# Kernel tuning notes

Measured on AMD Instinct MI355X. Metric: run time of the kernel, lower is better.

## Reference

```python
import jax, jax.numpy as jnp
import numpy as np

V = 30522   # bert-base-uncased vocab
E = 512     # embed_size
ATT = 512   # attention_dim
ENC = 2048  # encoder_dim
H = 512     # decoder_dim
B = 32
N = 49      # num image features (7x7)
T = 21      # caption length -> 20 decode steps


def setup_inputs() -> dict:
    key = jax.random.key(0)
    ks = jax.random.split(key, 12)
    s = lambda i, shape: jax.random.normal(ks[i], shape, jnp.float32) * 0.02
    features = jax.random.normal(ks[0], (B, N, ENC), jnp.float32)
    captions = jax.random.randint(ks[1], (B, T), 0, V, dtype=jnp.int32)
    return dict(
        features=features, captions=captions,
        emb=s(2, (V, E)),
        W_w=s(3, (ATT, H)), W_b=jnp.zeros((ATT,), jnp.float32),
        U_w=s(4, (ATT, ENC)), U_b=jnp.zeros((ATT,), jnp.float32),
        A_w=s(5, (1, ATT)), A_b=jnp.zeros((1,), jnp.float32),
        init_h_w=s(6, (H, ENC)), init_h_b=jnp.zeros((H,), jnp.float32),
        init_c_w=s(7, (H, ENC)), init_c_b=jnp.zeros((H,), jnp.float32),
        w_ih=s(8, (4 * H, E + ENC)), w_hh=s(9, (4 * H, H)),
        b_ih=jnp.zeros((4 * H,), jnp.float32), b_hh=jnp.zeros((4 * H,), jnp.float32),
        fcn_w=s(10, (V, H)), fcn_b=jnp.zeros((V,), jnp.float32),
    )


def reference(features, captions, emb, W_w, W_b, U_w, U_b, A_w, A_b,
              init_h_w, init_h_b, init_c_w, init_c_b,
              w_ih, w_hh, b_ih, b_hh, fcn_w, fcn_b):
    embeds = emb[captions]                      # [B, T, E]
    mean_f = features.mean(axis=1)              # [B, ENC]
    h0 = mean_f @ init_h_w.T + init_h_b         # [B, H]
    c0 = mean_f @ init_c_w.T + init_c_b
    # U(features) is h-independent: precompute once (same math as per-step in torch)
    u_hs = jnp.einsum('bne,ae->bna', features, U_w) + U_b  # [B, N, ATT]

    def step(carry, x_t):
        h, c = carry
        # Bahdanau attention
        w_ah = h @ W_w.T + W_b                               # [B, ATT]
        scores = jnp.tanh(u_hs + w_ah[:, None, :]) @ A_w[0] + A_b[0]  # [B, N]
        alpha = jax.nn.softmax(scores, axis=1)
        context = jnp.einsum('bn,bne->be', alpha, features)  # [B, ENC]
        # LSTMCell (torch gate order: i, f, g, o)
        lstm_in = jnp.concatenate([x_t, context], axis=1)    # [B, E+ENC]
        gates = lstm_in @ w_ih.T + b_ih + h @ w_hh.T + b_hh  # [B, 4H]
        i, f, g, o = jnp.split(gates, 4, axis=1)
        c2 = jax.nn.sigmoid(f) * c + jax.nn.sigmoid(i) * jnp.tanh(g)
        h2 = jax.nn.sigmoid(o) * jnp.tanh(c2)
        # dropout in eval mode = identity
        out = h2 @ fcn_w.T + fcn_b                           # [B, V]
        return (h2, c2), (out, alpha)

    xs = jnp.swapaxes(embeds[:, :-1], 0, 1)  # [T-1, B, E]
    _, (preds, alphas) = jax.lax.scan(step, (h0, c0), xs)
    return jnp.swapaxes(preds, 0, 1), jnp.swapaxes(alphas, 0, 1)
```

## Files before the change

### kernel.cpp

```cpp
#include <hip/hip_runtime.h>
#include <hip/hip_bf16.h>

#define VCB 30522
#define EMB 512
#define ATTD 512
#define ENC 2048
#define HD 512
#define BB 32
#define NF 49
#define TSTEPS 20
#define EIN 2560
#define KCAT 3072
#define WSTRIDE 3080
#define DTPB 512
#define NBLK 128

typedef __attribute__((ext_vector_type(8))) __bf16 bf16x8;
typedef __attribute__((ext_vector_type(4))) __bf16 bf16x4;
typedef __attribute__((ext_vector_type(4))) float floatx4;
typedef __hip_bfloat16 bf16;

__device__ __forceinline__ float bf2f(bf16 x){ return __bfloat162float(x); }
__device__ __forceinline__ bf16 f2bf(float x){ return __float2bfloat16(x); }
__device__ __forceinline__ float sigm(float x){ return 1.0f/(1.0f+expf(-x)); }
__device__ __forceinline__ float fast_tanh(float x){
    float e2 = __expf(2.0f*x);
    return 1.0f - 2.0f*__builtin_amdgcn_rcpf(e2 + 1.0f);
}

__device__ __forceinline__ unsigned coh_ld(const unsigned* p){
    return __hip_atomic_load(p, __ATOMIC_RELAXED, __HIP_MEMORY_SCOPE_AGENT);
}
__device__ __forceinline__ void coh_st(unsigned* p, unsigned v){
    __hip_atomic_store(p, v, __ATOMIC_RELAXED, __HIP_MEMORY_SCOPE_AGENT);
}
__device__ __forceinline__ unsigned pack2bf(float a, float b){
    unsigned short ua = __builtin_bit_cast(unsigned short, f2bf(a));
    unsigned short ub = __builtin_bit_cast(unsigned short, f2bf(b));
    return (unsigned)ua | ((unsigned)ub << 16);
}

__device__ __forceinline__ void gpost(unsigned* ctr){
    __syncthreads();
    if (threadIdx.x == 0)
        __hip_atomic_fetch_add(ctr, 1u, __ATOMIC_RELAXED, __HIP_MEMORY_SCOPE_AGENT);
}
__device__ __forceinline__ void gwait(const unsigned* ctr, unsigned tgt,
                                      volatile unsigned* sflag){
    float x = 1.0f;
    if (threadIdx.x < 64){
        while (coh_ld(ctr) < tgt){
#pragma unroll
            for (int i = 0; i < 8; ++i)
                x = __builtin_fmaf(x, 1.0000001f, 1e-12f);
        }
        if (threadIdx.x == 0) *sflag = tgt;
    } else {
        while (*sflag < tgt){
#pragma unroll
            for (int i = 0; i < 32; ++i)
                x = __builtin_fmaf(x, 1.0000001f, 1e-12f);
        }
    }
    asm volatile("" :: "v"(x));
    __syncthreads();
}

__device__ __forceinline__ float ld1(const void* base, size_t idx, int f){
    if (f) return ((const float*)base)[idx];
    return bf2f(((const bf16*)base)[idx]);
}
__device__ __forceinline__ bf16x8 ldbf8(const void* base, size_t idx, int f){
    if (f){
        const float* p = (const float*)base + idx;
        float4 a = *(const float4*)p, b = *(const float4*)(p+4);
        bf16x8 r;
        r[0]=(__bf16)a.x; r[1]=(__bf16)a.y; r[2]=(__bf16)a.z; r[3]=(__bf16)a.w;
        r[4]=(__bf16)b.x; r[5]=(__bf16)b.y; r[6]=(__bf16)b.z; r[7]=(__bf16)b.w;
        return r;
    }
    return *(const bf16x8*)((const bf16*)base + idx);
}
__device__ __forceinline__ bf16x8 bf8_of_f32(const float* p){
    float4 a = *(const float4*)p, b = *(const float4*)(p+4);
    bf16x8 r;
    r[0]=(__bf16)a.x; r[1]=(__bf16)a.y; r[2]=(__bf16)a.z; r[3]=(__bf16)a.w;
    r[4]=(__bf16)b.x; r[5]=(__bf16)b.y; r[6]=(__bf16)b.z; r[7]=(__bf16)b.w;
    return r;
}
__device__ __forceinline__ void st1(void* base, size_t idx, float v, int f){
    if (f) ((float*)base)[idx] = v;
    else   ((bf16*)base)[idx] = f2bf(v);
}

#define MFMA16(a,b,c) __builtin_amdgcn_mfma_f32_16x16x32_bf16(a,b,c,0,0,0)

__global__ void k_detect(const void* emb, int* flag, unsigned* bar){
    int tid = threadIdx.x;
    __shared__ int bad;
    if (tid == 0) bad = 0;
    for (int i = tid; i < 1024; i += 256) bar[i] = 0u;
    __syncthreads();
    const unsigned short* u = (const unsigned short*)emb;
    int local = 0;
    for (int i = tid; i < 4096; i += 256){
        int e = (u[i] >> 7) & 0xFF;
        if (e > 140) local = 1;
    }
    if (local) bad = 1;
    __syncthreads();
    if (tid == 0) *flag = bad;
}

__global__ void k_prep_gates(const void* w_ih, const void* w_hh, bf16* __restrict__ wcat,
                             const int* __restrict__ flag){
    int ff = *flag;
    int r = blockIdx.x, tid = threadIdx.x;
    for (int i = tid*8; i < KCAT; i += 2048){
        bf16x8 v;
        if (i + 8 <= EIN){
            v = ldbf8(w_ih, (size_t)r*EIN + i, ff);
        } else if (i >= EIN){
            v = ldbf8(w_hh, (size_t)r*HD + (i - EIN), ff);
        } else {
#pragma unroll
            for (int j = 0; j < 8; ++j){
                int k = i + j;
                v[j] = (__bf16)((k < EIN) ? ld1(w_ih, (size_t)r*EIN + k, ff)
                                          : ld1(w_hh, (size_t)r*HD + (k - EIN), ff));
            }
        }
        *(bf16x8*)(wcat + (size_t)r*KCAT + i) = v;
    }
}
__global__ void k_prep_cvt8(const void* src, bf16* __restrict__ dst, size_t n8,
                            const int* __restrict__ flag){
    int ff = *flag;
    size_t idx = (size_t)blockIdx.x*256 + threadIdx.x;
    size_t stride = (size_t)gridDim.x*256;
    for (size_t i = idx; i < n8; i += stride)
        *(bf16x8*)(dst + i*8) = ldbf8(src, i*8, ff);
}

__global__ void k_mean(const void* feat, float* __restrict__ mean_f,
                       const int* __restrict__ flag){
    int ff = *flag;
    int b = blockIdx.x, tid = threadIdx.x;
    for (int i = 0; i < ENC/256; ++i){
        int e = i*256 + tid;
        size_t base = (size_t)b*NF*ENC + e;
        float s = 0.f;
        for (int n = 0; n < NF; ++n) s += ld1(feat, base + (size_t)n*ENC, ff);
        mean_f[b*ENC + e] = s * (1.0f/49.0f);
    }
}

__global__ void k_init_hc(const float* __restrict__ mean_f,
                          const void* ihw, const void* ihb,
                          const void* icw, const void* icb,
                          float* __restrict__ Hbuf, float* __restrict__ c_f32,
                          const int* __restrict__ flag){
    int ff = *flag;
    int tid = threadIdx.x, wave = tid>>6, lane = tid&63, quad = lane>>4, lq = lane&15;
    int n0 = blockIdx.x*16;
    int ng = n0 + lq;
    const void* w = (ng < HD) ? ihw : icw;
    size_t wrow = (size_t)(ng < HD ? ng : ng - HD)*ENC;
    floatx4 acc[2] = {{0,0,0,0},{0,0,0,0}};
    int kb = wave*512;
    for (int kk = 0; kk < 16; ++kk){
        int k = kb + kk*32 + quad*8;
        bf16x8 bfr = ldbf8(w, wrow + k, ff);
#pragma unroll
        for (int mt = 0; mt < 2; ++mt){
            bf16x8 afr = bf8_of_f32(mean_f + (size_t)(mt*16+lq)*ENC + k);
            acc[mt] = MFMA16(afr, bfr, acc[mt]);
        }
    }
    __shared__ float red[4][2][16][16];
#pragma unroll
    for (int mt = 0; mt < 2; ++mt)
        for (int r = 0; r < 4; ++r)
            red[wave][mt][quad*4+r][lq] = acc[mt][r];
    __syncthreads();
    for (int rep = 0; rep < 2; ++rep){
        int idx = rep*256 + tid;
        int mt = idx>>8, mm = (idx>>4)&15, nn = idx&15;
        float v = red[0][mt][mm][nn]+red[1][mt][mm][nn]+red[2][mt][mm][nn]+red[3][mt][mm][nn];
        int n_g = n0 + nn, b = mt*16 + mm;
        if (n_g < HD) Hbuf[b*HD + n_g]        = v + ld1(ihb, n_g, ff);
        else          c_f32[b*HD + (n_g-HD)]  = v + ld1(icb, n_g - HD, ff);
    }
}

__global__ void k_uhs(const bf16* __restrict__ feat_bf, const void* U_w, const void* U_b,
                      float* __restrict__ u_hs, const int* __restrict__ flag){
    int ff = *flag;
    int tid = threadIdx.x, wave = tid>>6, lane = tid&63, quad = lane>>4, lq = lane&15;
    int m0 = blockIdx.x*16;
    int n0 = blockIdx.y*64 + wave*16;
    size_t arow = (size_t)(m0+lq)*ENC;
    size_t brow = (size_t)(n0+lq)*ENC;
    floatx4 acc = {0,0,0,0};
    for (int kk = 0; kk < ENC/32; ++kk){
        int k = kk*32 + quad*8;
        bf16x8 afr = *(const bf16x8*)(feat_bf + arow + k);
        bf16x8 bfr = ldbf8(U_w,  brow + k, ff);
        acc = MFMA16(afr, bfr, acc);
    }
    float ub = ld1(U_b, n0+lq, ff);
    for (int r = 0; r < 4; ++r){
        int m = m0 + quad*4 + r;
        u_hs[(size_t)m*ATTD + n0 + lq] = acc[r] + ub;
    }
}

__global__ void __launch_bounds__(DTPB) k_decode(
        float* __restrict__ Hbuf, const float* __restrict__ c0_f32,
        const bf16* __restrict__ Ww_bf, const void* __restrict__ W_b,
        const float* __restrict__ u_hs, const void* __restrict__ A_w,
        const void* __restrict__ A_b, const int* __restrict__ captions,
        const void* __restrict__ emb, const bf16* __restrict__ feat_bf,
        bf16* __restrict__ lstm_in, const bf16* __restrict__ wcat,
        const void* __restrict__ b_ih, const void* __restrict__ b_hh,
        bf16* __restrict__ Hall_bf, void* __restrict__ d_out,
        const int* __restrict__ flag, unsigned* __restrict__ bar)
{
    const int ff = *flag;
    const int bid = blockIdx.x, tid = threadIdx.x;
    const int wave = tid>>6, lane = tid&63, quad = lane>>4, lq = lane&15;

    __shared__ bf16  wlds[16*WSTRIDE];
    __shared__ float ubuf[4096];
    __shared__ float aw_s[ATTD];
    __shared__ float c_loc[BB*4];
    __shared__ float gbias[16];
    __shared__ unsigned sflag1, sflag2;

    unsigned* lin_u = (unsigned*)lstm_in;
    unsigned* flag1 = bar;
    unsigned* flag2 = bar + 64;

    if (tid == 0){ sflag1 = 0u; sflag2 = 0u; }

    for (int n = 0; n < 16; ++n){
        int g = n>>2, j = n&3;
        const bf16* src = wcat + (size_t)(g*HD + (bid<<2) + j)*KCAT;
        for (int c8 = tid; c8 < KCAT/8; c8 += DTPB)
            *(bf16x8*)(wlds + n*WSTRIDE + c8*8) = *(const bf16x8*)(src + c8*8);
    }
    if (tid < 128){
        int bb = tid&31, j = tid>>5, col = (bid<<2)+j;
        c_loc[bb*4+j] = c0_f32[bb*HD + col];
    }
    if (tid < 64){
        int bb = tid&31, j2 = tid>>5;
        int c0 = (bid<<2) + 2*j2;
        float h0 = Hbuf[bb*HD + c0], h1 = Hbuf[bb*HD + c0 + 1];
        coh_st(lin_u + (size_t)bb*(KCAT/2) + (EIN + c0)/2, pack2bf(h0, h1));
    }
    if (tid < 16){
        int g = tid>>2, j = tid&3, col = (bid<<2)+j;
        gbias[tid] = ld1(b_ih, g*HD+col, ff) + ld1(b_hh, g*HD+col, ff);
    }
    if (bid < BB)
        for (int i = tid; i < ATTD; i += DTPB) aw_s[i] = ld1(A_w, i, ff);
    gpost(flag2);

    float* h_sh    = ubuf;
    float* wah_s   = ubuf + 512;
    float* sc_s    = ubuf + 1024;
    float* alpha_s = ubuf + 1088;
    float (*red)[2][16][16] = (float (*)[2][16][16])ubuf;

    for (int t = 0; t < TSTEPS; ++t){
        if (bid < BB){
            gwait(flag2, 128u*(unsigned)(t+1), &sflag2);
            const int b = bid;
            const unsigned* hrow = (const unsigned*)(Hbuf + (size_t)t*BB*HD + b*HD);
            for (int i = tid; i < HD; i += DTPB)
                h_sh[i] = __uint_as_float(coh_ld(hrow + i));
            int cap = captions[b*21 + t];
            for (int e2 = tid; e2 < EMB/2; e2 += DTPB){
                float a = ld1(emb, (size_t)cap*EMB + 2*e2,     ff);
                float c = ld1(emb, (size_t)cap*EMB + 2*e2 + 1, ff);
                coh_st(lin_u + (size_t)b*(KCAT/2) + e2, pack2bf(a, c));
            }
            __syncthreads();
            for (int a = tid; a < ATTD; a += DTPB){
                const bf16* wr = Ww_bf + (size_t)a*HD;
                float s0=0.f, s1=0.f, s2=0.f, s3=0.f;
                for (int k = 0; k < HD; k += 8){
                    bf16x8 wv = *(const bf16x8*)(wr + k);
                    s0 += (float)wv[0]*h_sh[k+0] + (float)wv[4]*h_sh[k+4];
                    s1 += (float)wv[1]*h_sh[k+1] + (float)wv[5]*h_sh[k+5];
                    s2 += (float)wv[2]*h_sh[k+2] + (float)wv[6]*h_sh[k+6];
                    s3 += (float)wv[3]*h_sh[k+3] + (float)wv[7]*h_sh[k+7];
                }
                wah_s[a] = ((s0+s1)+(s2+s3)) + ld1(W_b, a, ff);
            }
            __syncthreads();
            {
                int a0 = lane*8;
                for (int n = wave; n < NF; n += 8){
                    const float* up = u_hs + (size_t)(b*NF + n)*ATTD + a0;
                    float4 u0 = *(const float4*)up;
                    float4 u1 = *(const float4*)(up + 4);
                    float p0 = fast_tanh(u0.x + wah_s[a0+0])*aw_s[a0+0]
                             + fast_tanh(u0.y + wah_s[a0+1])*aw_s[a0+1]
                             + fast_tanh(u0.z + wah_s[a0+2])*aw_s[a0+2]
                             + fast_tanh(u0.w + wah_s[a0+3])*aw_s[a0+3];
                    float p1 = fast_tanh(u1.x + wah_s[a0+4])*aw_s[a0+4]
                             + fast_tanh(u1.y + wah_s[a0+5])*aw_s[a0+5]
                             + fast_tanh(u1.z + wah_s[a0+6])*aw_s[a0+6]
                             + fast_tanh(u1.w + wah_s[a0+7])*aw_s[a0+7];
                    float p = p0 + p1;
                    for (int off = 32; off; off >>= 1) p += __shfl_down(p, off);
                    if (lane == 0) sc_s[n] = p + ld1(A_b, 0, ff);
                }
            }
            __syncthreads();
            if (wave == 0){
                float v = (lane < NF) ? sc_s[lane] : -1e30f;
                float mx = v;
                for (int off = 32; off; off >>= 1) mx = fmaxf(mx, __shfl_down(mx, off));
                mx = __shfl(mx, 0);
                float e = (lane < NF) ? expf(v - mx) : 0.f;
                float s = e;
                for (int off = 32; off; off >>= 1) s += __shfl_down(s, off);
                s = __shfl(s, 0);
                if (lane < NF){
                    float al = e / s;
                    alpha_s[lane] = al;
                    st1(d_out, (size_t)BB*TSTEPS*VCB + (size_t)b*(TSTEPS*NF) + t*NF + lane, al, ff);
                }
            }
            __syncthreads();
            {
                int e0 = tid*4;
                float acc[4] = {0,0,0,0};
#pragma unroll 7
                for (int n = 0; n < NF; ++n){
                    float al = alpha_s[n];
                    bf16x4 v = *(const bf16x4*)(feat_bf + (size_t)b*NF*ENC + (size_t)n*ENC + e0);
#pragma unroll
                    for (int j = 0; j < 4; ++j) acc[j] += al*(float)v[j];
                }
                unsigned* lrow = lin_u + (size_t)b*(KCAT/2) + (EMB + e0)/2;
                coh_st(lrow,     pack2bf(acc[0], acc[1]));
                coh_st(lrow + 1, pack2bf(acc[2], acc[3]));
            }
            gpost(flag1);
        }
        gwait(flag1, 32u*(unsigned)(t+1), &sflag1);

        {
            int kb = wave*384;
            floatx4 acc0 = {0,0,0,0}, acc1 = {0,0,0,0};
            const bf16* wrow = wlds + (size_t)lq*WSTRIDE;
            const unsigned* ar0 = lin_u + (size_t)lq*(KCAT/2);
            const unsigned* ar1 = lin_u + (size_t)(16+lq)*(KCAT/2);
            union U8 { unsigned u[4]; bf16x8 v; };
#pragma unroll
            for (int kk = 0; kk < 12; ++kk){
                int kd = (kb + kk*32 + quad*8) >> 1;
                bf16x8 bfr = *(const bf16x8*)(wrow + kb + kk*32 + quad*8);
                U8 a0, a1;
#pragma unroll
                for (int q = 0; q < 4; ++q){
                    a0.u[q] = coh_ld(ar0 + kd + q);
                    a1.u[q] = coh_ld(ar1 + kd + q);
                }
                acc0 = MFMA16(a0.v, bfr, acc0);
                acc1 = MFMA16(a1.v, bfr, acc1);
            }
#pragma unroll
            for (int r = 0; r < 4; ++r){
                red[wave][0][quad*4+r][lq] = acc0[r];
                red[wave][1][quad*4+r][lq] = acc1[r];
            }
        }
        __syncthreads();
        if (tid < 64){
            int bb = tid&31, j2 = tid>>5;
            int mt = bb>>4, mm = bb&15;
            float hn[2];
#pragma unroll
            for (int sub = 0; sub < 2; ++sub){
                int j = 2*j2 + sub;
                float G[4];
#pragma unroll
                for (int g = 0; g < 4; ++g){
                    int n = g*4 + j;
                    float s = 0.f;
#pragma unroll
                    for (int w8 = 0; w8 < 8; ++w8) s += red[w8][mt][mm][n];
                    G[g] = s + gbias[n];
                }
                float c_old = c_loc[bb*4+j];
                float c_new = sigm(G[1])*c_old + sigm(G[0])*tanhf(G[2]);
                float h_new = sigm(G[3])*tanhf(c_new);
                c_loc[bb*4+j] = c_new;
                hn[sub] = h_new;
            }
            int colb = (bid<<2) + 2*j2;
            unsigned* hb = (unsigned*)(Hbuf + (size_t)(t+1)*BB*HD + bb*HD + colb);
            coh_st(hb,     __float_as_uint(hn[0]));
            coh_st(hb + 1, __float_as_uint(hn[1]));
            ((unsigned*)Hall_bf)[((size_t)t*BB*HD + bb*HD + colb) >> 1] = pack2bf(hn[0], hn[1]);
            coh_st(lin_u + (size_t)bb*(KCAT/2) + (EIN + colb)/2, pack2bf(hn[0], hn[1]));
        }
        gpost(flag2);
    }
}

__global__ void __launch_bounds__(256) k_fcn(const bf16* __restrict__ Hall_bf,
                                             const bf16* __restrict__ fcnw_bf,
                                             const void* fcn_b, void* d_out,
                                             const int* __restrict__ flag){
    int ff = *flag;
    int tid = threadIdx.x, wave = tid>>6, lane = tid&63, quad = lane>>4, lq = lane&15;
    int n0 = blockIdx.x*64 + wave*16;
    int v = n0 + lq;
    int vc = (v < VCB) ? v : (VCB-1);
    const bf16* brow = fcnw_bf + (size_t)vc*HD;
    bf16x8 bfr[16];
#pragma unroll
    for (int kk = 0; kk < 16; ++kk) bfr[kk] = *(const bf16x8*)(brow + kk*32 + quad*8);
    float bias = ld1(fcn_b, vc, ff);
    for (int mt = 0; mt < 40; ++mt){
        const bf16* arow = Hall_bf + (size_t)(mt*16 + lq)*HD;
        floatx4 acc = {0,0,0,0};
#pragma unroll
        for (int kk = 0; kk < 16; ++kk){
            bf16x8 afr = *(const bf16x8*)(arow + kk*32 + quad*8);
            acc = MFMA16(afr, bfr[kk], acc);
        }
        if (v < VCB){
#pragma unroll
            for (int r = 0; r < 4; ++r){
                int m = mt*16 + quad*4 + r;
                int b = m & 31, tt = m >> 5;
                st1(d_out, (size_t)b*(TSTEPS*VCB) + (size_t)tt*VCB + v, acc[r] + bias, ff);
            }
        }
    }
}

extern "C" void kernel_launch(void* const* d_in, const int* in_sizes, int n_in,
                              void* d_out, int out_size, void* d_ws, size_t ws_size,
                              hipStream_t stream) {
    const void* feat  = d_in[0];
    const int*  caps  = (const int*)d_in[1];
    const void* emb   = d_in[2];
    const void* W_w   = d_in[3];
    const void* W_b   = d_in[4];
    const void* U_w   = d_in[5];
    const void* U_b   = d_in[6];
    const void* A_w   = d_in[7];
    const void* A_b   = d_in[8];
    const void* ihw   = d_in[9];
    const void* ihb   = d_in[10];
    const void* icw   = d_in[11];
    const void* icb   = d_in[12];
    const void* w_ih  = d_in[13];
    const void* w_hh  = d_in[14];
    const void* b_ih  = d_in[15];
    const void* b_hh  = d_in[16];
    const void* fcn_w = d_in[17];
    const void* fcn_b = d_in[18];

    char* ws = (char*)d_ws;
    size_t off = 0;
    float* u_hs    = (float*)(ws + off); off += (size_t)BB*NF*ATTD*4;
    float* c_f32   = (float*)(ws + off); off += (size_t)BB*HD*4;
    float* mean_f  = (float*)(ws + off); off += (size_t)BB*ENC*4;
    float* Hbuf    = (float*)(ws + off); off += (size_t)(TSTEPS+1)*BB*HD*4;
    bf16*  lstm_in = (bf16*) (ws + off); off += (size_t)BB*KCAT*2;
    bf16*  Hall_bf = (bf16*) (ws + off); off += (size_t)TSTEPS*BB*HD*2;
    bf16*  wcat    = (bf16*) (ws + off); off += (size_t)4*HD*KCAT*2;
    bf16*  fcnw_bf = (bf16*) (ws + off); off += (size_t)VCB*HD*2;
    bf16*  Ww_bf   = (bf16*) (ws + off); off += (size_t)ATTD*HD*2;
    bf16*  feat_bf = (bf16*) (ws + off); off += (size_t)BB*NF*ENC*2;
    int*   flag    = (int*)  (ws + off); off += 256;
    unsigned* bar  = (unsigned*)(ws + off); off += 4096;
    if (ws_size < off) return;

    k_detect    <<<1, 256, 0, stream>>>(emb, flag, bar);
    k_prep_gates<<<2048, 256, 0, stream>>>(w_ih, w_hh, wcat, flag);
    k_prep_cvt8 <<<2048, 256, 0, stream>>>(fcn_w, fcnw_bf, (size_t)VCB*HD/8, flag);
    k_prep_cvt8 <<<128, 256, 0, stream>>>(W_w, Ww_bf, (size_t)ATTD*HD/8, flag);
    k_prep_cvt8 <<<1024, 256, 0, stream>>>(feat, feat_bf, (size_t)BB*NF*ENC/8, flag);
    k_mean      <<<BB, 256, 0, stream>>>(feat, mean_f, flag);
    k_init_hc   <<<64, 256, 0, stream>>>(mean_f, ihw, ihb, icw, icb, Hbuf, c_f32, flag);
    k_uhs       <<<dim3(98, 8), 256, 0, stream>>>(feat_bf, U_w, U_b, u_hs, flag);

    {
        void* kargs[18] = {
            (void*)&Hbuf, (void*)&c_f32, (void*)&Ww_bf, (void*)&W_b,
            (void*)&u_hs, (void*)&A_w, (void*)&A_b, (void*)&caps,
            (void*)&emb, (void*)&feat_bf, (void*)&lstm_in, (void*)&wcat,
            (void*)&b_ih, (void*)&b_hh, (void*)&Hall_bf, (void*)&d_out,
            (void*)&flag, (void*)&bar
        };
        hipLaunchCooperativeKernel((void*)k_decode, dim3(NBLK), dim3(DTPB),
                                   kargs, 0, stream);
    }

    k_fcn<<<477, 256, 0, stream>>>(Hall_bf, fcnw_bf, fcn_b, d_out, flag);
}
```

Baseline: 1.577 ms.

## Distribute W·h attention GEMV and context reduction across blocks with extra grid flags

In the persistent decode kernel, the per-batch W_w·h GEMV moves from a scalar per-block loop to an MFMA computation split over 32 blocks, each owning 16 attention columns for all batches. The result is exchanged through a global buffer and a new flag. The alpha-weighted context sum is now spread over all 128 blocks (4 slices per batch) instead of 32, and the embedding copy is folded into that phase. This shortens the serial per-step work on the 32 attention blocks, but adds two more grid-wide barriers per step. It also drops the fp32 H buffer writes in favour of the bf16 copy already held in lstm_in.

Measured after the change: 1.451 ms. -7.9%, faster.

```diff
diff --git a/kernel.cpp b/kernel.cpp
--- a/kernel.cpp
+++ b/kernel.cpp
@@ -224,7 +224,8 @@
         bf16* __restrict__ lstm_in, const bf16* __restrict__ wcat,
         const void* __restrict__ b_ih, const void* __restrict__ b_hh,
         bf16* __restrict__ Hall_bf, void* __restrict__ d_out,
-        const int* __restrict__ flag, unsigned* __restrict__ bar)
+        const int* __restrict__ flag, unsigned* __restrict__ bar,
+        float* __restrict__ wah_u, float* __restrict__ alpha_u)
 {
     const int ff = *flag;
     const int bid = blockIdx.x, tid = threadIdx.x;
@@ -235,13 +236,17 @@
     __shared__ float aw_s[ATTD];
     __shared__ float c_loc[BB*4];
     __shared__ float gbias[16];
-    __shared__ unsigned sflag1, sflag2;
+    __shared__ unsigned sfW, sfS, sfL, sfH;
 
     unsigned* lin_u = (unsigned*)lstm_in;
-    unsigned* flag1 = bar;
-    unsigned* flag2 = bar + 64;
-
-    if (tid == 0){ sflag1 = 0u; sflag2 = 0u; }
+    unsigned* flagW = bar;
+    unsigned* flagS = bar + 64;
+    unsigned* flagL = bar + 128;
+    unsigned* flagH = bar + 192;
+    unsigned* wahu_u  = (unsigned*)wah_u;
+    unsigned* alphu_u = (unsigned*)alpha_u;
+
+    if (tid == 0){ sfW = 0u; sfS = 0u; sfL = 0u; sfH = 0u; }
 
     for (int n = 0; n < 16; ++n){
         int g = n>>2, j = n&3;
@@ -265,9 +270,8 @@
     }
     if (bid < BB)
         for (int i = tid; i < ATTD; i += DTPB) aw_s[i] = ld1(A_w, i, ff);
-    gpost(flag2);
-
-    float* h_sh    = ubuf;
+    gpost(flagH);
+
     float* wah_s   = ubuf + 512;
     float* sc_s    = ubuf + 1024;
     float* alpha_s = ubuf + 1088;
@@ -275,30 +279,50 @@
 
     for (int t = 0; t < TSTEPS; ++t){
         if (bid < BB){
-            gwait(flag2, 128u*(unsigned)(t+1), &sflag2);
+            gwait(flagH, 128u*(unsigned)(t+1), &sfH);
+            {
+                int n0 = bid<<4;
+                int kb = wave*64;
+                floatx4 acc0 = {0,0,0,0}, acc1 = {0,0,0,0};
+                const bf16* brow = Ww_bf + (size_t)(n0+lq)*HD;
+                union U8 { unsigned u[4]; bf16x8 v; };
+#pragma unroll
+                for (int kk = 0; kk < 2; ++kk){
+                    int k = kb + kk*32 + quad*8;
+                    bf16x8 bfr = *(const bf16x8*)(brow + k);
+                    U8 a0, a1;
+                    const unsigned* ar0 = lin_u + (size_t)lq*(KCAT/2) + (EIN+k)/2;
+                    const unsigned* ar1 = lin_u + (size_t)(16+lq)*(KCAT/2) + (EIN+k)/2;
+#pragma unroll
+                    for (int q = 0; q < 4; ++q){
+                        a0.u[q] = coh_ld(ar0 + q);
+                        a1.u[q] = coh_ld(ar1 + q);
+                    }
+                    acc0 = MFMA16(a0.v, bfr, acc0);
+                    acc1 = MFMA16(a1.v, bfr, acc1);
+                }
+#pragma unroll
+                for (int r = 0; r < 4; ++r){
+                    red[wave][0][quad*4+r][lq] = acc0[r];
+                    red[wave][1][quad*4+r][lq] = acc1[r];
+                }
+            }
+            __syncthreads();
+            {
+                int b = tid>>4, c = tid&15;
+                int mt = b>>4, mm = b&15;
+                float s = 0.f;
+#pragma unroll
+                for (int w8 = 0; w8 < 8; ++w8) s += red[w8][mt][mm][c];
+                int col = (bid<<4) + c;
+                coh_st(wahu_u + (size_t)b*ATTD + col,
+                       __float_as_uint(s + ld1(W_b, col, ff)));
+            }
+            gpost(flagW);
+
+            gwait(flagW, 32u*(unsigned)(t+1), &sfW);
             const int b = bid;
-            const unsigned* hrow = (const unsigned*)(Hbuf + (size_t)t*BB*HD + b*HD);
-            for (int i = tid; i < HD; i += DTPB)
-                h_sh[i] = __uint_as_float(coh_ld(hrow + i));
-            int cap = captions[b*21 + t];
-            for (int e2 = tid; e2 < EMB/2; e2 += DTPB){
-                float a = ld1(emb, (size_t)cap*EMB + 2*e2,     ff);
-                float c = ld1(emb, (size_t)cap*EMB + 2*e2 + 1, ff);
-                coh_st(lin_u + (size_t)b*(KCAT/2) + e2, pack2bf(a, c));
-            }
-            __syncthreads();
-            for (int a = tid; a < ATTD; a += DTPB){
-                const bf16* wr = Ww_bf + (size_t)a*HD;
-                float s0=0.f, s1=0.f, s2=0.f, s3=0.f;
-                for (int k = 0; k < HD; k += 8){
-                    bf16x8 wv = *(const bf16x8*)(wr + k);
-                    s0 += (float)wv[0]*h_sh[k+0] + (float)wv[4]*h_sh[k+4];
-                    s1 += (float)wv[1]*h_sh[k+1] + (float)wv[5]*h_sh[k+5];
-                    s2 += (float)wv[2]*h_sh[k+2] + (float)wv[6]*h_sh[k+6];
-                    s3 += (float)wv[3]*h_sh[k+3] + (float)wv[7]*h_sh[k+7];
-                }
-                wah_s[a] = ((s0+s1)+(s2+s3)) + ld1(W_b, a, ff);
-            }
+            wah_s[tid] = __uint_as_float(coh_ld(wahu_u + (size_t)b*ATTD + tid));
             __syncthreads();
             {
                 int a0 = lane*8;
@@ -331,28 +355,40 @@
                 s = __shfl(s, 0);
                 if (lane < NF){
                     float al = e / s;
-                    alpha_s[lane] = al;
+                    coh_st(alphu_u + b*64 + lane, __float_as_uint(al));
                     st1(d_out, (size_t)BB*TSTEPS*VCB + (size_t)b*(TSTEPS*NF) + t*NF + lane, al, ff);
                 }
             }
+            gpost(flagS);
+        }
+        gwait(flagS, 32u*(unsigned)(t+1), &sfS);
+        {
+            const int b = bid>>2, sl = bid&3;
+            if (tid < NF) alpha_s[tid] = __uint_as_float(coh_ld(alphu_u + b*64 + tid));
             __syncthreads();
-            {
-                int e0 = tid*4;
-                float acc[4] = {0,0,0,0};
+            if (tid < 256){
+                int col = sl*512 + 2*tid;
+                const bf16* fb = feat_bf + (size_t)b*NF*ENC + col;
+                float a0 = 0.f, a1 = 0.f;
 #pragma unroll 7
                 for (int n = 0; n < NF; ++n){
+                    unsigned fv = *(const unsigned*)(fb + (size_t)n*ENC);
+                    float lo = __uint_as_float(fv << 16);
+                    float hi = __uint_as_float(fv & 0xffff0000u);
                     float al = alpha_s[n];
-                    bf16x4 v = *(const bf16x4*)(feat_bf + (size_t)b*NF*ENC + (size_t)n*ENC + e0);
-#pragma unroll
-                    for (int j = 0; j < 4; ++j) acc[j] += al*(float)v[j];
-                }
-                unsigned* lrow = lin_u + (size_t)b*(KCAT/2) + (EMB + e0)/2;
-                coh_st(lrow,     pack2bf(acc[0], acc[1]));
-                coh_st(lrow + 1, pack2bf(acc[2], acc[3]));
-            }
-            gpost(flag1);
-        }
-        gwait(flag1, 32u*(unsigned)(t+1), &sflag1);
+                    a0 += al*lo; a1 += al*hi;
+                }
+                coh_st(lin_u + (size_t)b*(KCAT/2) + (EMB+col)/2, pack2bf(a0, a1));
+            } else if (tid >= 448){
+                int cap = captions[b*21 + t];
+                int col = sl*128 + 2*(tid - 448);
+                coh_st(lin_u + (size_t)b*(KCAT/2) + col/2,
+                       pack2bf(ld1(emb, (size_t)cap*EMB + col,     ff),
+                               ld1(emb, (size_t)cap*EMB + col + 1, ff)));
+            }
+            gpost(flagL);
+        }
+        gwait(flagL, 128u*(unsigned)(t+1), &sfL);
 
         {
             int kb = wave*384;
@@ -404,13 +440,10 @@
                 hn[sub] = h_new;
             }
             int colb = (bid<<2) + 2*j2;
-            unsigned* hb = (unsigned*)(Hbuf + (size_t)(t+1)*BB*HD + bb*HD + colb);
-            coh_st(hb,     __float_as_uint(hn[0]));
-            coh_st(hb + 1, __float_as_uint(hn[1]));
             ((unsigned*)Hall_bf)[((size_t)t*BB*HD + bb*HD + colb) >> 1] = pack2bf(hn[0], hn[1]);
             coh_st(lin_u + (size_t)bb*(KCAT/2) + (EIN + colb)/2, pack2bf(hn[0], hn[1]));
         }
-        gpost(flag2);
+        gpost(flagH);
     }
 }
 
@@ -482,6 +515,8 @@
     bf16*  fcnw_bf = (bf16*) (ws + off); off += (size_t)VCB*HD*2;
     bf16*  Ww_bf   = (bf16*) (ws + off); off += (size_t)ATTD*HD*2;
     bf16*  feat_bf = (bf16*) (ws + off); off += (size_t)BB*NF*ENC*2;
+    float* wah_u   = (float*)(ws + off); off += (size_t)BB*ATTD*4;
+    float* alpha_u = (float*)(ws + off); off += (size_t)BB*64*4;
     int*   flag    = (int*)  (ws + off); off += 256;
     unsigned* bar  = (unsigned*)(ws + off); off += 4096;
     if (ws_size < off) return;
@@ -496,12 +531,12 @@
     k_uhs       <<<dim3(98, 8), 256, 0, stream>>>(feat_bf, U_w, U_b, u_hs, flag);
 
     {
-        void* kargs[18] = {
+        void* kargs[20] = {
             (void*)&Hbuf, (void*)&c_f32, (void*)&Ww_bf, (void*)&W_b,
             (void*)&u_hs, (void*)&A_w, (void*)&A_b, (void*)&caps,
             (void*)&emb, (void*)&feat_bf, (void*)&lstm_in, (void*)&wcat,
             (void*)&b_ih, (void*)&b_hh, (void*)&Hall_bf, (void*)&d_out,
-            (void*)&flag, (void*)&bar
+            (void*)&flag, (void*)&bar, (void*)&wah_u, (void*)&alpha_u
         };
         hipLaunchCooperativeKernel((void*)k_decode, dim3(NBLK), dim3(DTPB),
                                    kargs, 0, stream);
```
